# Performance work log

Hardware: AMD Instinct MI355X
Metric: run time of the kernel (lower is better)

The kernel has to match this reference:

```python
import jax, jax.numpy as jnp
import numpy as np

QMIN, QMAX = -128.0, 127.0  # int8 range


def _fake_int_cast(t):
    # Emulates .to(torch.int8) on an already-clamped float tensor:
    # truncation toward zero, then back to float.
    return jnp.trunc(t)


def setup_inputs() -> dict:
    key = jax.random.key(0)
    k_x, k_w, k_ws, k_is, k_b = jax.random.split(key, 5)
    B, S, IN, OUT = 4, 2048, 4096, 4096
    x = jax.random.normal(k_x, (B, S, IN), dtype=jnp.float32)
    # quant_weight buffer holds int8 values (stored here as fp32 integers),
    # produced by quantizing a dense fp weight with per-out-channel scales.
    weight_scale = jax.random.uniform(k_ws, (OUT, 1), dtype=jnp.float32, minval=0.005, maxval=0.02)
    w_fp = jax.random.normal(k_w, (OUT, IN), dtype=jnp.float32) * 0.02
    quant_weight = jnp.trunc(jnp.clip(w_fp / weight_scale, QMIN, QMAX))
    input_scale = jax.random.uniform(k_is, (1,), dtype=jnp.float32, minval=0.01, maxval=0.03)
    bias = jax.random.normal(k_b, (OUT,), dtype=jnp.float32)
    return {"x": x, "quant_weight": quant_weight, "weight_scale": weight_scale,
            "input_scale": input_scale, "bias": bias}


def reference(x, quant_weight, weight_scale, input_scale, bias):
    # quantize input: clamp(x/scale) -> int8 (trunc toward zero) -> float
    quant_input = _fake_int_cast(jnp.clip(x / input_scale, QMIN, QMAX))
    # int8 matmul performed in fp32: [B,S,IN] @ [OUT,IN]^T -> [B,S,OUT]
    quant_output = jnp.einsum("bsi,oi->bso", quant_input, quant_weight)
    # dequantize with combined per-out-channel scale, viewed [1,1,OUT]
    scale = (weight_scale * input_scale).reshape((1,) * (quant_output.ndim - 1) + (-1,))
    output = quant_output * scale
    output = output + bias
    return output
```

## Files before the change

### kernel.cpp

```cpp
#include <hip/hip_runtime.h>


using v4i = __attribute__((ext_vector_type(4))) int;

typedef const __attribute__((address_space(1))) signed char gc_t;
typedef __attribute__((address_space(3))) signed char lc_t;

constexpr int BM = 128;
constexpr int BN = 128;
constexpr int BK = 64;


__device__ __forceinline__ int quant4(const float4 f, float s) {
    int a = (int)fminf(fmaxf(f.x / s, -128.0f), 127.0f);
    int b = (int)fminf(fmaxf(f.y / s, -128.0f), 127.0f);
    int c = (int)fminf(fmaxf(f.z / s, -128.0f), 127.0f);
    int d = (int)fminf(fmaxf(f.w / s, -128.0f), 127.0f);
    return (a & 0xff) | ((b & 0xff) << 8) | ((c & 0xff) << 16) | ((d & 0xff) << 24);
}

__device__ __forceinline__ int pack4i(const float4 f) {
    return ((int)f.x & 0xff) | (((int)f.y & 0xff) << 8) |
           (((int)f.z & 0xff) << 16) | (((int)f.w & 0xff) << 24);
}

__global__ void quant_x_kernel(const float* __restrict__ x,
                               const float* __restrict__ scale,
                               int4* __restrict__ out, int n16) {
    const float s = scale[0];
    int i = blockIdx.x * blockDim.x + threadIdx.x;
    if (i >= n16) return;
    const float4* p = (const float4*)x + (size_t)i * 4;
    float4 f0 = p[0], f1 = p[1], f2 = p[2], f3 = p[3];
    int4 o;
    o.x = quant4(f0, s);
    o.y = quant4(f1, s);
    o.z = quant4(f2, s);
    o.w = quant4(f3, s);
    out[i] = o;
}

__global__ void quant_w_kernel(const float* __restrict__ w,
                               int4* __restrict__ out, int n16) {
    int i = blockIdx.x * blockDim.x + threadIdx.x;
    if (i >= n16) return;
    const float4* p = (const float4*)w + (size_t)i * 4;
    float4 f0 = p[0], f1 = p[1], f2 = p[2], f3 = p[3];
    int4 o;
    o.x = pack4i(f0);
    o.y = pack4i(f1);
    o.z = pack4i(f2);
    o.w = pack4i(f3);
    out[i] = o;
}


__global__ __launch_bounds__(256) void gemm_i8_kernel(
    const signed char* __restrict__ Aq,
    const signed char* __restrict__ Wq,
    const float* __restrict__ wscale,
    const float* __restrict__ iscale,
    const float* __restrict__ bias,
    float* __restrict__ C,
    int M, int N, int K)
{
    __shared__ signed char As[BM * BK];
    __shared__ signed char Bs[BN * BK];

    const int tid  = threadIdx.x;
    const int wave = tid >> 6;
    const int lane = tid & 63;
    const int wm   = (wave >> 1) * 64;
    const int wn   = (wave & 1) * 64;

    const int m0 = blockIdx.y * BM;
    const int n0 = blockIdx.x * BN;

    const int srow = lane >> 2;
    const int scol = (lane & 3) * 16;

    const int fr = lane & 15;
    const int fk = (lane >> 4) * 16;

    v4i acc[4][4];
#pragma unroll
    for (int i = 0; i < 4; ++i)
#pragma unroll
        for (int j = 0; j < 4; ++j) acc[i][j] = (v4i){0, 0, 0, 0};

    const size_t Kz = (size_t)K;
    for (int k0 = 0; k0 < K; k0 += BK) {
#pragma unroll
        for (int c = 0; c < 2; ++c) {
            const int r = wave * 32 + c * 16;
            const signed char* ga = Aq + (size_t)(m0 + r + srow) * Kz + (k0 + scol);
            __builtin_amdgcn_global_load_lds((gc_t*)ga, (lc_t*)(As + r * BK), 16, 0, 0);
            const signed char* gb = Wq + (size_t)(n0 + r + srow) * Kz + (k0 + scol);
            __builtin_amdgcn_global_load_lds((gc_t*)gb, (lc_t*)(Bs + r * BK), 16, 0, 0);
        }
        __syncthreads();

        v4i af[4], bf[4];
#pragma unroll
        for (int t = 0; t < 4; ++t)
            af[t] = *(const v4i*)(As + (wm + t * 16 + fr) * BK + fk);
#pragma unroll
        for (int t = 0; t < 4; ++t)
            bf[t] = *(const v4i*)(Bs + (wn + t * 16 + fr) * BK + fk);

#pragma unroll
        for (int mt = 0; mt < 4; ++mt)
#pragma unroll
            for (int nt = 0; nt < 4; ++nt)
                acc[mt][nt] = __builtin_amdgcn_mfma_i32_16x16x64_i8(
                    af[mt], bf[nt], acc[mt][nt], 0, 0, 0);
        __syncthreads();
    }

    const float is = iscale[0];
#pragma unroll
    for (int nt = 0; nt < 4; ++nt) {
        const int col = n0 + wn + nt * 16 + fr;
        const float sc = wscale[col] * is;
        const float bv = bias[col];
#pragma unroll
        for (int mt = 0; mt < 4; ++mt) {
            const int rbase = m0 + wm + mt * 16 + (lane >> 4) * 4;
#pragma unroll
            for (int r = 0; r < 4; ++r) {
                C[(size_t)(rbase + r) * N + col] = (float)acc[mt][nt][r] * sc + bv;
            }
        }
    }
}


extern "C" void kernel_launch(void* const* d_in, const int* in_sizes, int n_in,
                              void* d_out, int out_size, void* d_ws, size_t ws_size,
                              hipStream_t stream) {
    const float* x  = (const float*)d_in[0];
    const float* qw = (const float*)d_in[1];
    const float* ws = (const float*)d_in[2];
    const float* is = (const float*)d_in[3];
    const float* bs = (const float*)d_in[4];
    float* out = (float*)d_out;

    const int nx = in_sizes[0];
    const int nw = in_sizes[1];
    const int N  = in_sizes[4];
    const int K  = nw / N;
    const int M  = nx / K;

    signed char* xq = (signed char*)d_ws;
    signed char* wq = (signed char*)d_ws + (size_t)nx;

    quant_x_kernel<<<nx / 16 / 256, 256, 0, stream>>>(x, is, (int4*)xq, nx / 16);
    quant_w_kernel<<<nw / 16 / 256, 256, 0, stream>>>(qw, (int4*)wq, nw / 16);

    dim3 grid(N / BN, M / BM);
    gemm_i8_kernel<<<grid, 256, 0, stream>>>(xq, wq, ws, is, bs, out, M, N, K);
}
```

Measured before the change: 462.8 us.

## Double K tile to 128 with XOR-swizzled LDS layout and simpler quant kernels

Raises the GEMM K tile from 64 to 128 so each barrier pair covers two MFMA sub-steps. LDS rows are XOR-swizzled by chunk index so fragment reads avoid bank conflicts, and global pointers are hoisted and advanced each iteration. Occupancy is hinted with launch_bounds(256,4). The quantization kernels now have each thread handle one float4 for fully coalesced access, and LDS use per block doubles.

```diff
diff --git a/kernel.cpp b/kernel.cpp
--- a/kernel.cpp
+++ b/kernel.cpp
@@ -8,7 +8,7 @@
 
 constexpr int BM = 128;
 constexpr int BN = 128;
-constexpr int BK = 64;
+constexpr int BK = 128;
 
 
 __device__ __forceinline__ int quant4(const float4 f, float s) {
@@ -19,43 +19,26 @@
     return (a & 0xff) | ((b & 0xff) << 8) | ((c & 0xff) << 16) | ((d & 0xff) << 24);
 }
 
-__device__ __forceinline__ int pack4i(const float4 f) {
-    return ((int)f.x & 0xff) | (((int)f.y & 0xff) << 8) |
-           (((int)f.z & 0xff) << 16) | (((int)f.w & 0xff) << 24);
+__global__ void quant_x_kernel(const float4* __restrict__ x,
+                               const float* __restrict__ scale,
+                               int* __restrict__ out, int n4) {
+    const float s = scale[0];
+    int i = blockIdx.x * blockDim.x + threadIdx.x;
+    if (i >= n4) return;
+    out[i] = quant4(x[i], s);
 }
 
-__global__ void quant_x_kernel(const float* __restrict__ x,
-                               const float* __restrict__ scale,
-                               int4* __restrict__ out, int n16) {
-    const float s = scale[0];
+__global__ void quant_w_kernel(const float4* __restrict__ w,
+                               int* __restrict__ out, int n4) {
     int i = blockIdx.x * blockDim.x + threadIdx.x;
-    if (i >= n16) return;
-    const float4* p = (const float4*)x + (size_t)i * 4;
-    float4 f0 = p[0], f1 = p[1], f2 = p[2], f3 = p[3];
-    int4 o;
-    o.x = quant4(f0, s);
-    o.y = quant4(f1, s);
-    o.z = quant4(f2, s);
-    o.w = quant4(f3, s);
-    out[i] = o;
-}
-
-__global__ void quant_w_kernel(const float* __restrict__ w,
-                               int4* __restrict__ out, int n16) {
-    int i = blockIdx.x * blockDim.x + threadIdx.x;
-    if (i >= n16) return;
-    const float4* p = (const float4*)w + (size_t)i * 4;
-    float4 f0 = p[0], f1 = p[1], f2 = p[2], f3 = p[3];
-    int4 o;
-    o.x = pack4i(f0);
-    o.y = pack4i(f1);
-    o.z = pack4i(f2);
-    o.w = pack4i(f3);
-    out[i] = o;
+    if (i >= n4) return;
+    float4 f = w[i];
+    out[i] = ((int)f.x & 0xff) | (((int)f.y & 0xff) << 8) |
+             (((int)f.z & 0xff) << 16) | (((int)f.w & 0xff) << 24);
 }
 
 
-__global__ __launch_bounds__(256) void gemm_i8_kernel(
+__global__ __launch_bounds__(256, 4) void gemm_i8_kernel(
     const signed char* __restrict__ Aq,
     const signed char* __restrict__ Wq,
     const float* __restrict__ wscale,
@@ -76,11 +59,13 @@
     const int m0 = blockIdx.y * BM;
     const int n0 = blockIdx.x * BN;
 
-    const int srow = lane >> 2;
-    const int scol = (lane & 3) * 16;
+    const int srow = lane >> 3;
+    const int gchunk = (lane & 7) ^ srow;
 
     const int fr = lane & 15;
-    const int fk = (lane >> 4) * 16;
+    const int qh = lane >> 4;
+    const int coff0 = (((0 * 4) + qh) ^ (fr & 7)) * 16;
+    const int coff1 = (((1 * 4) + qh) ^ (fr & 7)) * 16;
 
     v4i acc[4][4];
 #pragma unroll
@@ -89,31 +74,40 @@
         for (int j = 0; j < 4; ++j) acc[i][j] = (v4i){0, 0, 0, 0};
 
     const size_t Kz = (size_t)K;
+    const signed char* pA = Aq + (size_t)(m0 + wave * 32 + srow) * Kz + gchunk * 16;
+    const signed char* pB = Wq + (size_t)(n0 + wave * 32 + srow) * Kz + gchunk * 16;
+    lc_t* lA = (lc_t*)(As + (wave * 32) * BK);
+    lc_t* lB = (lc_t*)(Bs + (wave * 32) * BK);
+
     for (int k0 = 0; k0 < K; k0 += BK) {
 #pragma unroll
-        for (int c = 0; c < 2; ++c) {
-            const int r = wave * 32 + c * 16;
-            const signed char* ga = Aq + (size_t)(m0 + r + srow) * Kz + (k0 + scol);
-            __builtin_amdgcn_global_load_lds((gc_t*)ga, (lc_t*)(As + r * BK), 16, 0, 0);
-            const signed char* gb = Wq + (size_t)(n0 + r + srow) * Kz + (k0 + scol);
-            __builtin_amdgcn_global_load_lds((gc_t*)gb, (lc_t*)(Bs + r * BK), 16, 0, 0);
+        for (int c = 0; c < 4; ++c) {
+            __builtin_amdgcn_global_load_lds((gc_t*)(pA + (size_t)(c * 8) * Kz),
+                                             lA + c * 8 * BK, 16, 0, 0);
+            __builtin_amdgcn_global_load_lds((gc_t*)(pB + (size_t)(c * 8) * Kz),
+                                             lB + c * 8 * BK, 16, 0, 0);
         }
+        pA += BK;
+        pB += BK;
         __syncthreads();
 
-        v4i af[4], bf[4];
 #pragma unroll
-        for (int t = 0; t < 4; ++t)
-            af[t] = *(const v4i*)(As + (wm + t * 16 + fr) * BK + fk);
+        for (int s = 0; s < 2; ++s) {
+            const int coff = s ? coff1 : coff0;
+            v4i af[4], bf[4];
 #pragma unroll
-        for (int t = 0; t < 4; ++t)
-            bf[t] = *(const v4i*)(Bs + (wn + t * 16 + fr) * BK + fk);
-
+            for (int t = 0; t < 4; ++t)
+                af[t] = *(const v4i*)(As + (wm + t * 16 + fr) * BK + coff);
 #pragma unroll
-        for (int mt = 0; mt < 4; ++mt)
+            for (int t = 0; t < 4; ++t)
+                bf[t] = *(const v4i*)(Bs + (wn + t * 16 + fr) * BK + coff);
 #pragma unroll
-            for (int nt = 0; nt < 4; ++nt)
-                acc[mt][nt] = __builtin_amdgcn_mfma_i32_16x16x64_i8(
-                    af[mt], bf[nt], acc[mt][nt], 0, 0, 0);
+            for (int mt = 0; mt < 4; ++mt)
+#pragma unroll
+                for (int nt = 0; nt < 4; ++nt)
+                    acc[mt][nt] = __builtin_amdgcn_mfma_i32_16x16x64_i8(
+                        af[mt], bf[nt], acc[mt][nt], 0, 0, 0);
+        }
         __syncthreads();
     }
 
@@ -125,7 +119,7 @@
         const float bv = bias[col];
 #pragma unroll
         for (int mt = 0; mt < 4; ++mt) {
-            const int rbase = m0 + wm + mt * 16 + (lane >> 4) * 4;
+            const int rbase = m0 + wm + mt * 16 + qh * 4;
 #pragma unroll
             for (int r = 0; r < 4; ++r) {
                 C[(size_t)(rbase + r) * N + col] = (float)acc[mt][nt][r] * sc + bv;
@@ -154,8 +148,10 @@
     signed char* xq = (signed char*)d_ws;
     signed char* wq = (signed char*)d_ws + (size_t)nx;
 
-    quant_x_kernel<<<nx / 16 / 256, 256, 0, stream>>>(x, is, (int4*)xq, nx / 16);
-    quant_w_kernel<<<nw / 16 / 256, 256, 0, stream>>>(qw, (int4*)wq, nw / 16);
+    quant_x_kernel<<<nx / 4 / 256, 256, 0, stream>>>(
+        (const float4*)x, is, (int*)xq, nx / 4);
+    quant_w_kernel<<<nw / 4 / 256, 256, 0, stream>>>(
+        (const float4*)qw, (int*)wq, nw / 4);
 
     dim3 grid(N / BN, M / BM);
     gemm_i8_kernel<<<grid, 256, 0, stream>>>(xq, wq, ws, is, bs, out, M, N, K);
```

After: 378.1 us. 18.3% less time.
